# Optimization experiments

Measured on AMD Instinct MI355X. Metric: run time of the kernel, lower is better.

Reference implementation:

```python
import jax, jax.numpy as jnp
import numpy as np

B, S, D = 4, 2048, 1024
H, DK = 16, 64
NEG = -1e9


def setup_inputs() -> dict:
    key = jax.random.key(0)
    ks = jax.random.split(key, 6)
    hidden_states = jax.random.normal(ks[0], (B, S, D), dtype=jnp.float32)
    # evidence-constrained mask: causal mask plus random evidence restriction
    causal = jnp.tril(jnp.ones((S, S), dtype=bool))
    evid = jax.random.bernoulli(ks[1], 0.7, (S, S))
    allowed = causal & (evid | jnp.eye(S, dtype=bool))  # diag always allowed
    attention_mask = jnp.where(allowed, 0.0, NEG).astype(jnp.float32)
    scale = 0.02
    Wq = jax.random.normal(ks[2], (H * DK, D), dtype=jnp.float32) * scale
    Wk = jax.random.normal(ks[3], (H * DK, D), dtype=jnp.float32) * scale
    Wv = jax.random.normal(ks[4], (H * DK, D), dtype=jnp.float32) * scale
    Wo = jax.random.normal(ks[5], (D, H * DK), dtype=jnp.float32) * scale
    return {"hidden_states": hidden_states, "attention_mask": attention_mask,
            "Wq": Wq, "Wk": Wk, "Wv": Wv, "Wo": Wo}


def reference(hidden_states, attention_mask, Wq, Wk, Wv, Wo):
    b, s, _ = hidden_states.shape
    # nn.Linear(bias=False): y = x @ W.T ; reshape to (B,H,S,DK)
    def proj(x, W):
        y = jnp.einsum('bsd,ed->bse', x, W)
        return y.reshape(b, s, H, DK).transpose(0, 2, 1, 3)
    q = proj(hidden_states, Wq)
    k = proj(hidden_states, Wk)
    v = proj(hidden_states, Wv)
    logits = jnp.einsum('bhqd,bhkd->bhqk', q, k) / jnp.sqrt(jnp.float32(DK))
    logits = logits + attention_mask[None, None, :, :]
    attn = jax.nn.softmax(logits, axis=-1)
    ctx = jnp.einsum('bhqk,bhkd->bhqd', attn, v)
    ctx = ctx.transpose(0, 2, 1, 3).reshape(b, s, H * DK)
    out = jnp.einsum('bse,de->bsd', ctx, Wo)
    return out
```

## Files before the change

kernel.cpp:

```cpp
#include <hip/hip_runtime.h>
#include <hip/hip_bf16.h>
#include <math.h>

#define B_  4
#define S_  2048
#define D_  1024
#define H_  16
#define DK_ 64
#define M_  (B_*S_)
#define E_  (H_*DK_)
#define LOG2E  1.4426950408889634f
#define QSCALE 0.18033688011112042f

typedef short  bf16x8 __attribute__((ext_vector_type(8)));
typedef float  f32x4  __attribute__((ext_vector_type(4)));
typedef unsigned short u16;

__device__ __forceinline__ u16 f2b(float x) {
    __hip_bfloat16 h = __float2bfloat16(x);
    return *(u16*)&h;
}

__device__ __forceinline__ void async16(const u16* g, u16* l) {
    __builtin_amdgcn_global_load_lds(
        (const __attribute__((address_space(1))) unsigned int*)g,
        (__attribute__((address_space(3))) unsigned int*)l, 16, 0, 0);
}

__global__ __launch_bounds__(256)
void cvt_x(const float* __restrict__ s, u16* __restrict__ d, int n8) {
    int i = blockIdx.x * 256 + threadIdx.x;
    if (i >= n8) return;
    const float4* s4 = (const float4*)s;
    float4 a = s4[2 * i], b = s4[2 * i + 1];
    u16 o[8] = {f2b(a.x), f2b(a.y), f2b(a.z), f2b(a.w),
                f2b(b.x), f2b(b.y), f2b(b.z), f2b(b.w)};
    *(uint4*)(d + (size_t)8 * i) = *(const uint4*)o;
}

__global__ __launch_bounds__(256)
void cvt_w4(const float* __restrict__ s0, const float* __restrict__ s1,
            const float* __restrict__ s2, const float* __restrict__ s3,
            u16* __restrict__ d0, u16* __restrict__ d1,
            u16* __restrict__ d2, u16* __restrict__ d3, int n8) {
    const float* s = blockIdx.y == 0 ? s0 : blockIdx.y == 1 ? s1 : blockIdx.y == 2 ? s2 : s3;
    u16*         d = blockIdx.y == 0 ? d0 : blockIdx.y == 1 ? d1 : blockIdx.y == 2 ? d2 : d3;
    int i = blockIdx.x * 256 + threadIdx.x;
    if (i >= n8) return;
    const float4* s4 = (const float4*)s;
    float4 a = s4[2 * i], b = s4[2 * i + 1];
    u16 o[8] = {f2b(a.x), f2b(a.y), f2b(a.z), f2b(a.w),
                f2b(b.x), f2b(b.y), f2b(b.z), f2b(b.w)};
    *(uint4*)(d + (size_t)8 * i) = *(const uint4*)o;
}

__device__ __forceinline__ void gemm_core(
    const u16* __restrict__ Ag, const u16* __restrict__ Bg, int K,
    int bm, int bn, u16* As, u16* Bs, f32x4 (&acc)[4][4])
{
    const int tid  = threadIdx.x;
    const int w    = tid >> 6, lane = tid & 63;
    const int l15  = lane & 15, quad = lane >> 4;
    const int wm   = (w >> 1) * 64, wn = (w & 1) * 64;
    const int srow = lane >> 3;
    const int sg   = (lane & 7) ^ srow;
    const int sx   = l15 & 7;

    for (int k0 = 0; k0 < K; k0 += 64) {
        __syncthreads();
        #pragma unroll
        for (int i = 0; i < 4; i++) {
            const int row = w * 32 + i * 8 + srow;
            async16(Ag + (size_t)(bm + row) * K + k0 + sg * 8,
                    As + (size_t)(w * 32 + i * 8) * 64);
            async16(Bg + (size_t)(bn + row) * K + k0 + sg * 8,
                    Bs + (size_t)(w * 32 + i * 8) * 64);
        }
        __syncthreads();

        #pragma unroll
        for (int s = 0; s < 2; s++) {
            bf16x8 af[4], bf[4];
            #pragma unroll
            for (int i = 0; i < 4; i++)
                af[i] = *(const bf16x8*)(As + (size_t)(wm + i * 16 + l15) * 64
                                            + (((s * 4 + quad) ^ sx) * 8));
            #pragma unroll
            for (int j = 0; j < 4; j++)
                bf[j] = *(const bf16x8*)(Bs + (size_t)(wn + j * 16 + l15) * 64
                                            + (((s * 4 + quad) ^ sx) * 8));
            #pragma unroll
            for (int i = 0; i < 4; i++)
                #pragma unroll
                for (int j = 0; j < 4; j++)
                    acc[i][j] = __builtin_amdgcn_mfma_f32_16x16x32_bf16(af[i], bf[j], acc[i][j], 0, 0, 0);
        }
    }
}

__global__ __launch_bounds__(256)
void gemm_qkv(const u16* __restrict__ Xb,
              const u16* __restrict__ Wqb, const u16* __restrict__ Wkb,
              const u16* __restrict__ Wvb,
              u16* __restrict__ Qm, u16* __restrict__ Km, u16* __restrict__ Vt)
{
    __shared__ u16 As[128 * 64];
    __shared__ u16 Bs[128 * 64];
    const int bm    = blockIdx.x * 128;
    const int nb    = blockIdx.y;
    const int which = nb >> 3;
    const int col0  = (nb & 7) * 128;
    const u16* Bg = which == 0 ? Wqb : which == 1 ? Wkb : Wvb;

    f32x4 acc[4][4] = {};
    gemm_core(Xb, Bg, D_, bm, col0, As, Bs, acc);

    const int tid = threadIdx.x;
    const int w   = tid >> 6, lane = tid & 63;
    const int l15 = lane & 15, quad = lane >> 4;
    const int wm  = (w >> 1) * 64, wn = (w & 1) * 64;

    if (which == 2) {
        #pragma unroll
        for (int i = 0; i < 4; i++)
            #pragma unroll
            for (int j = 0; j < 4; j++) {
                int c    = col0 + wn + j * 16 + l15;
                int tok0 = bm + wm + i * 16 + quad * 4;
                u16 pk[4] = {f2b(acc[i][j][0]), f2b(acc[i][j][1]),
                             f2b(acc[i][j][2]), f2b(acc[i][j][3])};
                size_t idx = (((size_t)((tok0 >> 11) * E_ + c)) << 11) + (tok0 & 2047);
                *(uint2*)(Vt + idx) = *(const uint2*)pk;
            }
    } else {
        u16* Cm = which == 0 ? Qm : Km;
        const float sc = which == 0 ? QSCALE : 1.0f;
        #pragma unroll
        for (int i = 0; i < 4; i++)
            #pragma unroll
            for (int j = 0; j < 4; j++)
                #pragma unroll
                for (int r = 0; r < 4; r++) {
                    int row = bm + wm + i * 16 + quad * 4 + r;
                    int c   = col0 + wn + j * 16 + l15;
                    Cm[(size_t)row * E_ + c] = f2b(acc[i][j][r] * sc);
                }
    }
}

__global__ __launch_bounds__(256)
void gemm_out(const u16* __restrict__ Cmx, const u16* __restrict__ Wob,
              float* __restrict__ out)
{
    __shared__ u16 As[128 * 64];
    __shared__ u16 Bs[128 * 64];
    const int bm = blockIdx.x * 128;
    const int bn = blockIdx.y * 128;

    f32x4 acc[4][4] = {};
    gemm_core(Cmx, Wob, E_, bm, bn, As, Bs, acc);

    const int tid = threadIdx.x;
    const int w   = tid >> 6, lane = tid & 63;
    const int l15 = lane & 15, quad = lane >> 4;
    const int wm  = (w >> 1) * 64, wn = (w & 1) * 64;
    #pragma unroll
    for (int i = 0; i < 4; i++)
        #pragma unroll
        for (int j = 0; j < 4; j++)
            #pragma unroll
            for (int r = 0; r < 4; r++)
                out[(size_t)(bm + wm + i * 16 + quad * 4 + r) * D_ + bn + wn + j * 16 + l15]
                    = acc[i][j][r];
}

__global__ __launch_bounds__(256)
void flash_attn(const u16* __restrict__ Q, const u16* __restrict__ Kc,
                const u16* __restrict__ Vt, const float* __restrict__ mask,
                u16* __restrict__ ctx)
{
    const int bh  = blockIdx.x;
    const int qt  = (gridDim.y - 1) - blockIdx.y;
    const int b   = bh >> 4, h = bh & 15;
    const int tid = threadIdx.x;
    const int w   = tid >> 6, lane = tid & 63;
    const int l15 = lane & 15, quad = lane >> 4;
    const int q0  = qt * 64;

    __shared__ u16 Ks[64 * 64];
    __shared__ u16 Vs[64 * 64];
    __shared__ u16 Ps[4][16 * 64];

    const u16* qbase = Q + ((size_t)(b * S_ + q0 + w * 16 + l15)) * E_ + h * DK_;
    bf16x8 qf0 = *(const bf16x8*)(qbase + quad * 8);
    bf16x8 qf1 = *(const bf16x8*)(qbase + 32 + quad * 8);

    f32x4 acc[4] = {};
    float lsum = 0.f;

    const int sr  = lane >> 3;
    const int sg  = (lane & 7) ^ sr;
    const int sx  = l15 & 7;
    const float* mptr = mask + (size_t)(q0 + w * 16 + l15) * S_ + quad * 4;
    u16* Pw = &Ps[w][0];

    for (int kt = 0; kt <= qt; ++kt) {
        const int k0 = kt * 64;

        float4 mk[4];
        #pragma unroll
        for (int t = 0; t < 4; t++)
            mk[t] = *(const float4*)(mptr + k0 + t * 16);

        __syncthreads();
        #pragma unroll
        for (int i = 0; i < 2; i++) {
            const int row8 = w * 16 + i * 8;
            async16(Kc + ((size_t)(b * S_ + k0 + row8 + sr)) * E_ + h * DK_ + sg * 8,
                    Ks + row8 * 64);
            async16(Vt + ((size_t)(bh * DK_ + row8 + sr)) * S_ + k0 + sg * 8,
                    Vs + row8 * 64);
        }
        __syncthreads();

        f32x4 st[4] = {};
        #pragma unroll
        for (int t = 0; t < 4; t++) {
            bf16x8 kf0 = *(const bf16x8*)(Ks + (t * 16 + l15) * 64 + ((quad ^ sx) * 8));
            bf16x8 kf1 = *(const bf16x8*)(Ks + (t * 16 + l15) * 64 + (((4 + quad) ^ sx) * 8));
            st[t] = __builtin_amdgcn_mfma_f32_16x16x32_bf16(kf0, qf0, st[t], 0, 0, 0);
            st[t] = __builtin_amdgcn_mfma_f32_16x16x32_bf16(kf1, qf1, st[t], 0, 0, 0);
        }

        #pragma unroll
        for (int t = 0; t < 4; t++) {
            float p0 = exp2f(fmaf(mk[t].x, LOG2E, st[t][0]));
            float p1 = exp2f(fmaf(mk[t].y, LOG2E, st[t][1]));
            float p2 = exp2f(fmaf(mk[t].z, LOG2E, st[t][2]));
            float p3 = exp2f(fmaf(mk[t].w, LOG2E, st[t][3]));
            lsum += (p0 + p1) + (p2 + p3);
            u16 pk[4] = {f2b(p0), f2b(p1), f2b(p2), f2b(p3)};
            *(uint2*)(Pw + l15 * 64 + (((2 * t + (quad >> 1)) ^ sx) * 8) + (quad & 1) * 4)
                = *(const uint2*)pk;
        }

        #pragma unroll
        for (int s = 0; s < 2; s++) {
            bf16x8 pf = *(const bf16x8*)(Pw + l15 * 64 + (((4 * s + quad) ^ sx) * 8));
            #pragma unroll
            for (int nt = 0; nt < 4; nt++) {
                bf16x8 vf = *(const bf16x8*)(Vs + (nt * 16 + l15) * 64 + (((4 * s + quad) ^ sx) * 8));
                acc[nt] = __builtin_amdgcn_mfma_f32_16x16x32_bf16(pf, vf, acc[nt], 0, 0, 0);
            }
        }
    }

    lsum += __shfl_xor(lsum, 16, 64);
    lsum += __shfl_xor(lsum, 32, 64);
    float linv = 1.0f / lsum;
    float ir[4];
    #pragma unroll
    for (int r = 0; r < 4; r++) ir[r] = __shfl(linv, quad * 4 + r, 16);
    #pragma unroll
    for (int r = 0; r < 4; r++) {
        size_t orow = ((size_t)(b * S_ + q0 + w * 16 + quad * 4 + r)) * E_ + h * DK_;
        #pragma unroll
        for (int nt = 0; nt < 4; nt++)
            ctx[orow + nt * 16 + l15] = f2b(acc[nt][r] * ir[r]);
    }
}

extern "C" void kernel_launch(void* const* d_in, const int* in_sizes, int n_in,
                              void* d_out, int out_size, void* d_ws, size_t ws_size,
                              hipStream_t stream) {
    const float* X    = (const float*)d_in[0];
    const float* mask = (const float*)d_in[1];
    const float* Wq   = (const float*)d_in[2];
    const float* Wk   = (const float*)d_in[3];
    const float* Wv   = (const float*)d_in[4];
    const float* Wo   = (const float*)d_in[5];
    float* out = (float*)d_out;

    char* p = (char*)d_ws;
    u16* Qm  = (u16*)p; p += (size_t)M_ * E_ * 2;
    u16* Km  = (u16*)p; p += (size_t)M_ * E_ * 2;
    u16* Vt  = (u16*)p; p += (size_t)M_ * E_ * 2;
    u16* Wqb = (u16*)p; p += (size_t)E_ * D_ * 2;
    u16* Wkb = (u16*)p; p += (size_t)E_ * D_ * 2;
    u16* Wvb = (u16*)p; p += (size_t)E_ * D_ * 2;
    u16* Wob = (u16*)p; p += (size_t)D_ * E_ * 2;
    u16* Xb  = (u16*)p;
    u16* Cm  = Xb;

    cvt_x<<<(M_ * D_ / 8 + 255) / 256, 256, 0, stream>>>(X, Xb, M_ * D_ / 8);
    cvt_w4<<<dim3(E_ * D_ / 8 / 256, 4), 256, 0, stream>>>(Wq, Wk, Wv, Wo,
                                                           Wqb, Wkb, Wvb, Wob, E_ * D_ / 8);

    gemm_qkv<<<dim3(M_ / 128, 24), 256, 0, stream>>>(Xb, Wqb, Wkb, Wvb, Qm, Km, Vt);

    flash_attn<<<dim3(B_ * H_, S_ / 64), 256, 0, stream>>>(Qm, Km, Vt, mask, Cm);

    gemm_out<<<dim3(M_ / 128, D_ / 128), 256, 0, stream>>>(Cm, Wob, out);
}
```

Before: 287.4 us.

## Double query tile per block and double-buffer K/V loads in flash attention

Each block now covers 128 query rows instead of 64, with each wave owning two 16-row sub-tiles. Every K/V fragment read from LDS therefore feeds twice as many MFMAs, and half as many blocks re-stream the same K/V data. K and V tiles are double-buffered: the next tile's async load is issued while the current tile is computed, so the loop needs one barrier per iteration instead of two. The cost is more registers per thread (two sets of accumulators and scores), more LDS, and half as many blocks to balance the causal triangle across CUs.

```diff
diff --git a/kernel.cpp b/kernel.cpp
--- a/kernel.cpp
+++ b/kernel.cpp
@@ -185,88 +185,116 @@
     const int tid = threadIdx.x;
     const int w   = tid >> 6, lane = tid & 63;
     const int l15 = lane & 15, quad = lane >> 4;
-    const int q0  = qt * 64;
-
-    __shared__ u16 Ks[64 * 64];
-    __shared__ u16 Vs[64 * 64];
-    __shared__ u16 Ps[4][16 * 64];
-
-    const u16* qbase = Q + ((size_t)(b * S_ + q0 + w * 16 + l15)) * E_ + h * DK_;
-    bf16x8 qf0 = *(const bf16x8*)(qbase + quad * 8);
-    bf16x8 qf1 = *(const bf16x8*)(qbase + 32 + quad * 8);
-
-    f32x4 acc[4] = {};
-    float lsum = 0.f;
-
-    const int sr  = lane >> 3;
-    const int sg  = (lane & 7) ^ sr;
-    const int sx  = l15 & 7;
-    const float* mptr = mask + (size_t)(q0 + w * 16 + l15) * S_ + quad * 4;
-    u16* Pw = &Ps[w][0];
-
-    for (int kt = 0; kt <= qt; ++kt) {
-        const int k0 = kt * 64;
-
-        float4 mk[4];
-        #pragma unroll
-        for (int t = 0; t < 4; t++)
-            mk[t] = *(const float4*)(mptr + k0 + t * 16);
-
+    const int q0  = qt * 128;
+    const int nkt = 2 * qt + 2;
+
+    __shared__ u16 Ks[2][64 * 64];
+    __shared__ u16 Vs[2][64 * 64];
+    __shared__ u16 Ps[4][2][16 * 64];
+
+    bf16x8 qf[2][2];
+    #pragma unroll
+    for (int s = 0; s < 2; s++) {
+        const u16* qb = Q + ((size_t)(b * S_ + q0 + w * 32 + s * 16 + l15)) * E_ + h * DK_;
+        qf[s][0] = *(const bf16x8*)(qb + quad * 8);
+        qf[s][1] = *(const bf16x8*)(qb + 32 + quad * 8);
+    }
+
+    f32x4 acc[2][4] = {};
+    float lsum[2] = {0.f, 0.f};
+
+    const int sr = lane >> 3;
+    const int sg = (lane & 7) ^ sr;
+    const int sx = l15 & 7;
+
+    #pragma unroll
+    for (int i = 0; i < 2; i++) {
+        const int row8 = w * 16 + i * 8;
+        async16(Kc + ((size_t)(b * S_ + row8 + sr)) * E_ + h * DK_ + sg * 8,
+                &Ks[0][row8 * 64]);
+        async16(Vt + ((size_t)(bh * DK_ + row8 + sr)) * S_ + sg * 8,
+                &Vs[0][row8 * 64]);
+    }
+
+    for (int kt = 0; kt < nkt; ++kt) {
+        const int k0  = kt * 64;
+        const int buf = kt & 1;
         __syncthreads();
-        #pragma unroll
-        for (int i = 0; i < 2; i++) {
-            const int row8 = w * 16 + i * 8;
-            async16(Kc + ((size_t)(b * S_ + k0 + row8 + sr)) * E_ + h * DK_ + sg * 8,
-                    Ks + row8 * 64);
-            async16(Vt + ((size_t)(bh * DK_ + row8 + sr)) * S_ + k0 + sg * 8,
-                    Vs + row8 * 64);
-        }
-        __syncthreads();
-
-        f32x4 st[4] = {};
+
+        f32x4 st[2][4] = {};
         #pragma unroll
         for (int t = 0; t < 4; t++) {
-            bf16x8 kf0 = *(const bf16x8*)(Ks + (t * 16 + l15) * 64 + ((quad ^ sx) * 8));
-            bf16x8 kf1 = *(const bf16x8*)(Ks + (t * 16 + l15) * 64 + (((4 + quad) ^ sx) * 8));
-            st[t] = __builtin_amdgcn_mfma_f32_16x16x32_bf16(kf0, qf0, st[t], 0, 0, 0);
-            st[t] = __builtin_amdgcn_mfma_f32_16x16x32_bf16(kf1, qf1, st[t], 0, 0, 0);
-        }
-
-        #pragma unroll
-        for (int t = 0; t < 4; t++) {
-            float p0 = exp2f(fmaf(mk[t].x, LOG2E, st[t][0]));
-            float p1 = exp2f(fmaf(mk[t].y, LOG2E, st[t][1]));
-            float p2 = exp2f(fmaf(mk[t].z, LOG2E, st[t][2]));
-            float p3 = exp2f(fmaf(mk[t].w, LOG2E, st[t][3]));
-            lsum += (p0 + p1) + (p2 + p3);
-            u16 pk[4] = {f2b(p0), f2b(p1), f2b(p2), f2b(p3)};
-            *(uint2*)(Pw + l15 * 64 + (((2 * t + (quad >> 1)) ^ sx) * 8) + (quad & 1) * 4)
-                = *(const uint2*)pk;
+            bf16x8 kf0 = *(const bf16x8*)(&Ks[buf][(t * 16 + l15) * 64 + ((quad ^ sx) * 8)]);
+            bf16x8 kf1 = *(const bf16x8*)(&Ks[buf][(t * 16 + l15) * 64 + (((4 + quad) ^ sx) * 8)]);
+            st[0][t] = __builtin_amdgcn_mfma_f32_16x16x32_bf16(kf0, qf[0][0], st[0][t], 0, 0, 0);
+            st[0][t] = __builtin_amdgcn_mfma_f32_16x16x32_bf16(kf1, qf[0][1], st[0][t], 0, 0, 0);
+            st[1][t] = __builtin_amdgcn_mfma_f32_16x16x32_bf16(kf0, qf[1][0], st[1][t], 0, 0, 0);
+            st[1][t] = __builtin_amdgcn_mfma_f32_16x16x32_bf16(kf1, qf[1][1], st[1][t], 0, 0, 0);
+        }
+
+        if (kt + 1 < nkt) {
+            const int k1 = k0 + 64, nb = buf ^ 1;
+            #pragma unroll
+            for (int i = 0; i < 2; i++) {
+                const int row8 = w * 16 + i * 8;
+                async16(Kc + ((size_t)(b * S_ + k1 + row8 + sr)) * E_ + h * DK_ + sg * 8,
+                        &Ks[nb][row8 * 64]);
+                async16(Vt + ((size_t)(bh * DK_ + row8 + sr)) * S_ + k1 + sg * 8,
+                        &Vs[nb][row8 * 64]);
+            }
         }
 
         #pragma unroll
         for (int s = 0; s < 2; s++) {
-            bf16x8 pf = *(const bf16x8*)(Pw + l15 * 64 + (((4 * s + quad) ^ sx) * 8));
+            const float* mp = mask + (size_t)(q0 + w * 32 + s * 16 + l15) * S_ + k0 + quad * 4;
+            float4 mk[4];
+            #pragma unroll
+            for (int t = 0; t < 4; t++) mk[t] = *(const float4*)(mp + t * 16);
+            u16* Pw = &Ps[w][s][0];
+            float ls = 0.f;
+            #pragma unroll
+            for (int t = 0; t < 4; t++) {
+                float p0 = exp2f(fmaf(mk[t].x, LOG2E, st[s][t][0]));
+                float p1 = exp2f(fmaf(mk[t].y, LOG2E, st[s][t][1]));
+                float p2 = exp2f(fmaf(mk[t].z, LOG2E, st[s][t][2]));
+                float p3 = exp2f(fmaf(mk[t].w, LOG2E, st[s][t][3]));
+                ls += (p0 + p1) + (p2 + p3);
+                u16 pk[4] = {f2b(p0), f2b(p1), f2b(p2), f2b(p3)};
+                *(uint2*)(Pw + l15 * 64 + (((2 * t + (quad >> 1)) ^ sx) * 8) + (quad & 1) * 4)
+                    = *(const uint2*)pk;
+            }
+            lsum[s] += ls;
+        }
+
+        #pragma unroll
+        for (int sb = 0; sb < 2; sb++) {
+            bf16x8 pf0 = *(const bf16x8*)(&Ps[w][0][l15 * 64 + (((4 * sb + quad) ^ sx) * 8)]);
+            bf16x8 pf1 = *(const bf16x8*)(&Ps[w][1][l15 * 64 + (((4 * sb + quad) ^ sx) * 8)]);
             #pragma unroll
             for (int nt = 0; nt < 4; nt++) {
-                bf16x8 vf = *(const bf16x8*)(Vs + (nt * 16 + l15) * 64 + (((4 * s + quad) ^ sx) * 8));
-                acc[nt] = __builtin_amdgcn_mfma_f32_16x16x32_bf16(pf, vf, acc[nt], 0, 0, 0);
+                bf16x8 vf = *(const bf16x8*)(&Vs[buf][(nt * 16 + l15) * 64 + (((4 * sb + quad) ^ sx) * 8)]);
+                acc[0][nt] = __builtin_amdgcn_mfma_f32_16x16x32_bf16(pf0, vf, acc[0][nt], 0, 0, 0);
+                acc[1][nt] = __builtin_amdgcn_mfma_f32_16x16x32_bf16(pf1, vf, acc[1][nt], 0, 0, 0);
             }
         }
     }
 
-    lsum += __shfl_xor(lsum, 16, 64);
-    lsum += __shfl_xor(lsum, 32, 64);
-    float linv = 1.0f / lsum;
-    float ir[4];
     #pragma unroll
-    for (int r = 0; r < 4; r++) ir[r] = __shfl(linv, quad * 4 + r, 16);
-    #pragma unroll
-    for (int r = 0; r < 4; r++) {
-        size_t orow = ((size_t)(b * S_ + q0 + w * 16 + quad * 4 + r)) * E_ + h * DK_;
-        #pragma unroll
-        for (int nt = 0; nt < 4; nt++)
-            ctx[orow + nt * 16 + l15] = f2b(acc[nt][r] * ir[r]);
+    for (int s = 0; s < 2; s++) {
+        float ls = lsum[s];
+        ls += __shfl_xor(ls, 16, 64);
+        ls += __shfl_xor(ls, 32, 64);
+        float linv = 1.0f / ls;
+        float ir[4];
+        #pragma unroll
+        for (int r = 0; r < 4; r++) ir[r] = __shfl(linv, quad * 4 + r, 16);
+        #pragma unroll
+        for (int r = 0; r < 4; r++) {
+            size_t orow = ((size_t)(b * S_ + q0 + w * 32 + s * 16 + quad * 4 + r)) * E_ + h * DK_;
+            #pragma unroll
+            for (int nt = 0; nt < 4; nt++)
+                ctx[orow + nt * 16 + l15] = f2b(acc[s][nt][r] * ir[r]);
+        }
     }
 }
 
@@ -298,7 +326,7 @@
 
     gemm_qkv<<<dim3(M_ / 128, 24), 256, 0, stream>>>(Xb, Wqb, Wkb, Wvb, Qm, Km, Vt);
 
-    flash_attn<<<dim3(B_ * H_, S_ / 64), 256, 0, stream>>>(Qm, Km, Vt, mask, Cm);
+    flash_attn<<<dim3(B_ * H_, S_ / 128), 256, 0, stream>>>(Qm, Km, Vt, mask, Cm);
 
     gemm_out<<<dim3(M_ / 128, D_ / 128), 256, 0, stream>>>(Cm, Wob, out);
 }
```

New measurement: 306.6 us. 1.07x slower.
